# Performance work log

Measured on AMD Instinct MI355X. Metric: run time of the kernel, lower is better.

## Reference

```python
import jax, jax.numpy as jnp
import numpy as np

B, N, DIM = 1, 4096, 512
HEADS, LOCAL_HEADS = 8, 4           # int(8*0.6)=4 local, 4 content
CONTENT_HEADS = HEADS - LOCAL_HEADS
HEAD_DIM = DIM // HEADS             # 64
WINDOW = 64                         # == H == W so window attention is well-formed
TOPK_RATIO = 0.2
SCALE = HEAD_DIM ** -0.5


def _window_partition(x, ws):
    Bb, H, W, C = x.shape
    pad_h = (ws - H % ws) % ws
    pad_w = (ws - W % ws) % ws
    x = jnp.pad(x, ((0, 0), (0, pad_h), (0, pad_w), (0, 0)))
    Hp, Wp = H + pad_h, W + pad_w
    x = x.reshape(Bb, Hp // ws, ws, Wp // ws, ws, C)
    win = x.transpose(0, 1, 3, 2, 4, 5).reshape(-1, ws, ws, C)
    return win, (Hp, Wp)


def _window_unpartition(win, ws, pad_hw, hw):
    Hp, Wp = pad_hw
    H, W = hw
    Bb = win.shape[0] // (Hp * Wp // ws // ws)
    x = win.reshape(Bb, Hp // ws, Wp // ws, ws, ws, -1)
    x = x.transpose(0, 1, 3, 2, 4, 5).reshape(Bb, Hp, Wp, -1)
    return x[:, :H, :W, :]


def setup_inputs() -> dict:
    key = jax.random.key(0)
    ks = jax.random.split(key, 12)
    s = 0.02
    f32 = jnp.float32
    ld = LOCAL_HEADS * HEAD_DIM      # 256
    cd = CONTENT_HEADS * HEAD_DIM    # 256
    return {
        'x': jax.random.normal(ks[0], (B, N, DIM), f32),
        'W_lqkv': jax.random.normal(ks[1], (DIM, 3 * ld), f32) * s,
        'b_lqkv': jnp.zeros((3 * ld,), f32),
        'W_cqkv': jax.random.normal(ks[2], (DIM, 3 * cd), f32) * s,
        'b_cqkv': jnp.zeros((3 * cd,), f32),
        'W_lproj': jax.random.normal(ks[3], (ld, DIM), f32) * s,
        'b_lproj': jnp.zeros((DIM,), f32),
        'W_cproj': jax.random.normal(ks[4], (cd, DIM), f32) * s,
        'b_cproj': jnp.zeros((DIM,), f32),
        'W_s1': jax.random.normal(ks[5], (DIM, DIM // 2), f32) * s,
        'b_s1': jnp.zeros((DIM // 2,), f32),
        'W_s2': jax.random.normal(ks[6], (DIM // 2, 1), f32) * s,
        'b_s2': jnp.zeros((1,), f32),
    }


def reference(x, W_lqkv, b_lqkv, W_cqkv, b_cqkv, W_lproj, b_lproj,
              W_cproj, b_cproj, W_s1, b_s1, W_s2, b_s2):
    Bb, Nn, C = x.shape
    H = W = int(np.sqrt(Nn))

    # ---- local (windowed) attention branch ----
    x_sp = x.reshape(Bb, H, W, C)
    x_win, pad_hw = _window_partition(x_sp, WINDOW)           # (Bw, ws, ws, C)
    Bw, Hw, Ww, _ = x_win.shape
    Nw = Hw * Ww
    xl = x_win.reshape(Bw, Nw, C)
    lqkv = (xl @ W_lqkv + b_lqkv).reshape(Bw, Nw, 3, LOCAL_HEADS, HEAD_DIM)
    lqkv = lqkv.transpose(2, 0, 3, 1, 4)                      # (3, Bw, h, Nw, d)
    lq, lk, lv = lqkv[0], lqkv[1], lqkv[2]
    lattn = jnp.einsum('bhqd,bhkd->bhqk', lq, lk) * SCALE
    lattn = jax.nn.softmax(lattn, axis=-1)
    lo = jnp.einsum('bhqk,bhkd->bhqd', lattn, lv)
    lo = lo.transpose(0, 2, 1, 3).reshape(Bw, Hw, Ww, LOCAL_HEADS * HEAD_DIM)
    lo = _window_unpartition(lo, WINDOW, pad_hw, (H, W)).reshape(Bb, Nn, -1)
    local_x = lo @ W_lproj + b_lproj

    # ---- saliency-gated content-based sparse attention branch ----
    h = jax.nn.gelu(x @ W_s1 + b_s1, approximate=False)
    scores = (h @ W_s2 + b_s2)[..., 0]                        # (B, N)
    K = max(1, int(Nn * TOPK_RATIO))
    _, idx = jax.lax.top_k(scores, K)                         # (B, K)
    mask = jnp.zeros((Bb, Nn), bool).at[jnp.arange(Bb)[:, None], idx].set(True)

    cqkv = (x @ W_cqkv + b_cqkv).reshape(Bb, Nn, 3, CONTENT_HEADS, HEAD_DIM)
    cqkv = cqkv.transpose(2, 0, 3, 1, 4)
    cq, ck, cv = cqkv[0], cqkv[1], cqkv[2]
    cattn = jnp.einsum('bhqd,bhkd->bhqk', cq, ck) * SCALE
    cattn = jnp.where(mask[:, None, None, :], cattn, -jnp.inf)
    cattn = jax.nn.softmax(cattn, axis=-1)
    co = jnp.einsum('bhqk,bhkd->bhqd', cattn, cv)
    co = co.transpose(0, 2, 1, 3).reshape(Bb, Nn, CONTENT_HEADS * HEAD_DIM)
    content_x = co @ W_cproj + b_cproj

    out = local_x + content_x
    attn = jnp.concatenate([lattn.mean(axis=1), cattn.mean(axis=1)], axis=1)
    return out, attn
```

## Files before the change

kernel.cpp:

```cpp
#include <hip/hip_runtime.h>

typedef __bf16 bf16;
typedef __bf16 bf16x8 __attribute__((ext_vector_type(8)));
typedef float  floatx4 __attribute__((ext_vector_type(4)));

__device__ __forceinline__ floatx4 mfma16(bf16x8 a, bf16x8 b, floatx4 c) {
    return __builtin_amdgcn_mfma_f32_16x16x32_bf16(a, b, c, 0, 0, 0);
}

__global__ void k_transpose(const float* __restrict__ src, bf16* __restrict__ dst,
                            int R, int C) {
    __shared__ float tile[32][33];
    int c0 = blockIdx.x * 32, r0 = blockIdx.y * 32;
    int tx = threadIdx.x, ty = threadIdx.y;
    for (int i = ty; i < 32; i += 8) {
        int r = r0 + i, c = c0 + tx;
        tile[i][tx] = (r < R && c < C) ? src[r * C + c] : 0.f;
    }
    __syncthreads();
    for (int i = ty; i < 32; i += 8) {
        int r = r0 + tx, c = c0 + i;
        if (r < R && c < C) dst[(size_t)c * R + r] = (bf16)tile[tx][i];
    }
}

__global__ __launch_bounds__(256) void k_xcast(const float* __restrict__ x,
                                               bf16* __restrict__ xb) {
    int i = (blockIdx.x * 256 + threadIdx.x) * 8;
    float4 f0 = *(const float4*)(x + i);
    float4 f1 = *(const float4*)(x + i + 4);
    bf16x8 a;
    a[0] = (bf16)f0.x; a[1] = (bf16)f0.y; a[2] = (bf16)f0.z; a[3] = (bf16)f0.w;
    a[4] = (bf16)f1.x; a[5] = (bf16)f1.y; a[6] = (bf16)f1.z; a[7] = (bf16)f1.w;
    *(bf16x8*)(xb + i) = a;
}

__global__ __launch_bounds__(256) void k_vtr(const bf16* __restrict__ src,
                                             bf16* __restrict__ dst, int R) {
    __shared__ bf16 tile[64][66];
    int t = threadIdx.x;
    int tr = blockIdx.x, h = blockIdx.y;
    const bf16* s = src + ((size_t)h * R + tr * 64) * 64;
    #pragma unroll
    for (int rr = 0; rr < 16; ++rr) {
        int row = rr * 4 + (t >> 6);
        tile[row][t & 63] = s[row * 64 + (t & 63)];
    }
    __syncthreads();
    bf16* d = dst + (size_t)h * 64 * R + tr * 64;
    #pragma unroll
    for (int cc = 0; cc < 16; ++cc) {
        int col = cc * 4 + (t >> 6);
        d[(size_t)col * R + (t & 63)] = tile[t & 63][col];
    }
}

__global__ __launch_bounds__(256) void k_qkv(
    const bf16* __restrict__ xb,
    const bf16* __restrict__ WlT, const bf16* __restrict__ WcT,
    const float* __restrict__ b_l, const float* __restrict__ b_c,
    bf16* __restrict__ lq, bf16* __restrict__ lk, bf16* __restrict__ lv,
    bf16* __restrict__ cq, bf16* __restrict__ ck, bf16* __restrict__ cv)
{
    const int tid = threadIdx.x;
    const int wave = tid >> 6, lane = tid & 63;
    const int ln15 = lane & 15, quad = lane >> 4;
    const int m0 = blockIdx.x * 64 + wave * 16;
    const int n0 = blockIdx.y * 64;

    floatx4 acc[4];
    for (int s = 0; s < 4; ++s) acc[s] = (floatx4){0.f, 0.f, 0.f, 0.f};

    for (int k0 = 0; k0 < 512; k0 += 32) {
        bf16x8 a = *(const bf16x8*)(xb + (m0 + ln15) * 512 + k0 + quad * 8);
        for (int s = 0; s < 4; ++s) {
            int cg = n0 + s * 16 + ln15;
            const bf16* bt = (cg < 768) ? (WlT + cg * 512) : (WcT + (cg - 768) * 512);
            bf16x8 b = *(const bf16x8*)(bt + k0 + quad * 8);
            acc[s] = mfma16(a, b, acc[s]);
        }
    }

    for (int s = 0; s < 4; ++s) {
        int cg = n0 + s * 16 + ln15;
        for (int r = 0; r < 4; ++r) {
            int row = m0 + quad * 4 + r;
            float v = acc[s][r];
            if (cg < 768) {
                v += b_l[cg];
                int qkv = cg >> 8, hh = (cg >> 6) & 3, d = cg & 63;
                if (qkv == 0)      lq[(hh * 4096 + row) * 64 + d] = (bf16)(v * 0.125f);
                else if (qkv == 1) lk[(hh * 4096 + row) * 64 + d] = (bf16)v;
                else               lv[(hh * 4096 + row) * 64 + d] = (bf16)v;
            } else {
                int c = cg - 768;
                v += b_c[c];
                int qkv = c >> 8, hh = (c >> 6) & 3, d = c & 63;
                if (qkv == 0)      cq[(hh * 4096 + row) * 64 + d] = (bf16)(v * 0.125f);
                else if (qkv == 1) ck[(hh * 4096 + row) * 64 + d] = (bf16)v;
                else               cv[(hh * 4096 + row) * 64 + d] = (bf16)v;
            }
        }
    }
}

__global__ __launch_bounds__(256) void k_scores(
    const float* __restrict__ x, const float* __restrict__ Ws1,
    const float* __restrict__ bs1, const float* __restrict__ Ws2,
    const float* __restrict__ bs2, float* __restrict__ scores)
{
    __shared__ float xs[4][512];
    int row0 = blockIdx.x * 4;
    int t = threadIdx.x;
    for (int i = t; i < 512; i += 256) {
        int r = i >> 7, k4 = (i & 127) * 4;
        *(float4*)&xs[r][k4] = *(const float4*)&x[(row0 + r) * 512 + k4];
    }
    __syncthreads();
    int r = t >> 6, cb = (t & 63) * 4;
    float acc[4] = {0.f, 0.f, 0.f, 0.f};
    #pragma unroll 4
    for (int k = 0; k < 512; ++k) {
        float a = xs[r][k];
        float4 w = *(const float4*)(Ws1 + k * 256 + cb);
        acc[0] = fmaf(a, w.x, acc[0]); acc[1] = fmaf(a, w.y, acc[1]);
        acc[2] = fmaf(a, w.z, acc[2]); acc[3] = fmaf(a, w.w, acc[3]);
    }
    float s = 0.f;
    for (int j = 0; j < 4; ++j) {
        float v = acc[j] + bs1[cb + j];
        float g = 0.5f * v * (1.0f + erff(v * 0.70710678118654752f));
        s = fmaf(g, Ws2[cb + j], s);
    }
    s += __shfl_xor(s, 1, 64);  s += __shfl_xor(s, 2, 64);
    s += __shfl_xor(s, 4, 64);  s += __shfl_xor(s, 8, 64);
    s += __shfl_xor(s, 16, 64); s += __shfl_xor(s, 32, 64);
    if ((t & 63) == 0) scores[row0 + r] = s + bs2[0];
}

__global__ __launch_bounds__(1024) void k_topk(const float* __restrict__ scores,
                                               int* __restrict__ sel, int* __restrict__ pos) {
    __shared__ unsigned ubuf[4096];
    __shared__ unsigned cga[2048], cgb[2048];
    __shared__ int bidx[1024];
    __shared__ int ctr, bctr, Bbin;
    int tid = threadIdx.x;
    if (tid == 0) { ctr = 0; bctr = 0; }
    for (int i = tid; i < 2048; i += 1024) cga[i] = 0u;
    __syncthreads();
    for (int i = tid; i < 4096; i += 1024) {
        unsigned s = __float_as_uint(scores[i]);
        unsigned u = (s & 0x80000000u) ? ~s : (s | 0x80000000u);
        ubuf[i] = u;
        pos[i] = -1;
        atomicAdd(&cga[u >> 21], 1u);
    }
    __syncthreads();
    unsigned* src = cga; unsigned* dst = cgb;
    for (int off = 1; off < 2048; off <<= 1) {
        for (int i = tid; i < 2048; i += 1024)
            dst[i] = src[i] + ((i + off < 2048) ? src[i + off] : 0u);
        __syncthreads();
        unsigned* tmp = src; src = dst; dst = tmp;
    }
    for (int b = tid; b < 2048; b += 1024) {
        unsigned ge = src[b];
        unsigned gt = (b < 2047) ? src[b + 1] : 0u;
        if (ge >= 819u && gt < 819u) Bbin = b;
    }
    __syncthreads();
    int B = Bbin;
    int countAbove = (B < 2047) ? (int)src[B + 1] : 0;
    int need = 819 - countAbove;
    for (int i = tid; i < 4096; i += 1024) {
        int b = (int)(ubuf[i] >> 21);
        if (b > B) {
            int slot = atomicAdd(&ctr, 1);
            sel[slot] = i;
            pos[i] = slot;
        } else if (b == B) {
            int ls = atomicAdd(&bctr, 1);
            if (ls < 1024) bidx[ls] = i;
        }
    }
    __syncthreads();
    int m = bctr;
    if (m <= 1024) {
        for (int e = tid; e < m; e += 1024) {
            int i = bidx[e];
            unsigned ui = ubuf[i];
            int rank = 0;
            for (int j = 0; j < m; ++j) {
                int ij = bidx[j];
                unsigned uj = ubuf[ij];
                rank += (uj > ui || (uj == ui && ij < i)) ? 1 : 0;
            }
            if (rank < need) { int slot = countAbove + rank; sel[slot] = i; pos[i] = slot; }
        }
    } else {
        for (int i = tid; i < 4096; i += 1024) {
            if ((int)(ubuf[i] >> 21) != B) continue;
            unsigned ui = ubuf[i];
            int rank = 0;
            for (int j = 0; j < 4096; ++j) {
                if ((int)(ubuf[j] >> 21) != B) continue;
                unsigned uj = ubuf[j];
                rank += (uj > ui || (uj == ui && j < i)) ? 1 : 0;
            }
            if (rank < need) { int slot = countAbove + rank; sel[slot] = i; pos[i] = slot; }
        }
    }
}

__global__ __launch_bounds__(256) void k_gather(
    const bf16* __restrict__ ck, const bf16* __restrict__ cv,
    const int* __restrict__ sel,
    bf16* __restrict__ ckg, bf16* __restrict__ cvg)
{
    int g = blockIdx.x * 4 + (threadIdx.x >> 6);
    int d = threadIdx.x & 63;
    int hh = g / 896, r = g % 896;
    int src = (r < 819) ? sel[r] : -1;
    bf16 kv = (src >= 0) ? ck[(hh * 4096 + src) * 64 + d] : (bf16)0.0f;
    bf16 vv = (src >= 0) ? cv[(hh * 4096 + src) * 64 + d] : (bf16)0.0f;
    ckg[(hh * 896 + r) * 64 + d] = kv;
    cvg[(hh * 896 + r) * 64 + d] = vv;
}

__global__ __launch_bounds__(256, 5) void k_pass2b(
    const bf16* __restrict__ lq, const bf16* __restrict__ lk, const bf16* __restrict__ lvT,
    const bf16* __restrict__ cq, const bf16* __restrict__ ckg, const bf16* __restrict__ cvgT,
    float* __restrict__ partOL,
    float* __restrict__ partOC,
    float* __restrict__ partSL,
    float* __restrict__ partSC)
{
    __shared__ __align__(16) bf16 pbuf[4][2][16 * 40];
    int wave = threadIdx.x >> 6, lane = threadIdx.x & 63;
    int ln15 = lane & 15, quad = lane >> 4;
    int m0 = blockIdx.x * 64 + wave * 16;
    int y = blockIdx.y;
    bool local = y < 32;
    int h     = local ? (y >> 3) : ((y - 32) >> 1);
    int split = local ? (y & 7) : ((y - 32) & 1);
    int NV    = local ? 4096 : 896;
    int kbeg  = local ? split * 512 : split * 448;
    int kcnt  = local ? 512 : 448;

    const bf16* Qh = (local ? lq : cq) + (h * 4096 + m0) * 64;
    const bf16* Kh = (local ? lk : ckg) + h * NV * 64;
    const bf16* Vh = (local ? lvT : cvgT) + h * 64 * NV;

    bf16x8 af0 = *(const bf16x8*)(Qh + ln15 * 64 + quad * 8);
    bf16x8 af1 = *(const bf16x8*)(Qh + ln15 * 64 + 32 + quad * 8);

    floatx4 o[4];
    #pragma unroll
    for (int ds = 0; ds < 4; ++ds) o[ds] = (floatx4){0.f, 0.f, 0.f, 0.f};
    float se[4] = {0.f, 0.f, 0.f, 0.f};

    for (int key0 = kbeg; key0 < kbeg + kcnt; key0 += 64) {
        #pragma unroll
        for (int c = 0; c < 2; ++c) {
            int kb = key0 + c * 32;
            bf16* pb = &pbuf[wave][c][0];
            #pragma unroll
            for (int s = 0; s < 2; ++s) {
                int kc = kb + s * 16;
                const bf16* krow = Kh + (kc + ln15) * 64;
                floatx4 z0 = (floatx4){0.f, 0.f, 0.f, 0.f};
                floatx4 z1 = (floatx4){0.f, 0.f, 0.f, 0.f};
                z0 = mfma16(af0, *(const bf16x8*)(krow + quad * 8), z0);
                z1 = mfma16(af1, *(const bf16x8*)(krow + 32 + quad * 8), z1);
                bool valid = local || (kc + ln15) < 819;
                #pragma unroll
                for (int r = 0; r < 4; ++r) {
                    float p = valid ? __expf(fminf(z0[r] + z1[r], 60.f)) : 0.0f;
                    se[r] += p;
                    pb[(quad * 4 + r) * 40 + s * 16 + ln15] = (bf16)p;
                }
            }
        }
        #pragma unroll
        for (int c = 0; c < 2; ++c) {
            int kb = key0 + c * 32;
            bf16x8 ap = *(const bf16x8*)(&pbuf[wave][c][0] + ln15 * 40 + quad * 8);
            #pragma unroll
            for (int ds = 0; ds < 4; ++ds) {
                const bf16* vrow = Vh + (ds * 16 + ln15) * NV + kb + quad * 8;
                o[ds] = mfma16(ap, *(const bf16x8*)vrow, o[ds]);
            }
        }
    }

    float* ps = (local ? partSL : partSC) + (split * 4 + h) * 4096;
    #pragma unroll
    for (int r = 0; r < 4; ++r) {
        float s = se[r];
        s += __shfl_xor(s, 1, 64);
        s += __shfl_xor(s, 2, 64);
        s += __shfl_xor(s, 4, 64);
        s += __shfl_xor(s, 8, 64);
        if (ln15 == 0) ps[m0 + quad * 4 + r] = s;
    }

    float* ob = (local ? partOL : partOC) + (size_t)split * (4096 * 256);
    #pragma unroll
    for (int ds = 0; ds < 4; ++ds)
        for (int r = 0; r < 4; ++r)
            ob[(m0 + quad * 4 + r) * 256 + h * 64 + ds * 16 + ln15] = o[ds][r];
}

__global__ __launch_bounds__(256) void k_reduce2(
    const float* __restrict__ partOL, const float* __restrict__ partOC,
    const float* __restrict__ partSL, const float* __restrict__ partSC,
    float* __restrict__ lsum, float* __restrict__ lo, float* __restrict__ co)
{
    int t = threadIdx.x;
    int q0 = blockIdx.x * 4;
    int r = t >> 6, cc = (t & 63) * 4;
    int q = q0 + r;
    int h = cc >> 6;

    float sl = 0.f;
    #pragma unroll
    for (int s = 0; s < 8; ++s) sl += partSL[(s * 4 + h) * 4096 + q];
    float rll = 1.0f / fmaxf(sl, 1e-30f);
    float a0 = 0.f, a1 = 0.f, a2 = 0.f, a3 = 0.f;
    #pragma unroll
    for (int s = 0; s < 8; ++s) {
        float4 v = *(const float4*)(partOL + (size_t)s * 1048576 + q * 256 + cc);
        a0 += v.x; a1 += v.y; a2 += v.z; a3 += v.w;
    }
    *(float4*)(lo + q * 256 + cc) = (float4){a0 * rll, a1 * rll, a2 * rll, a3 * rll};

    float sc = partSC[h * 4096 + q] + partSC[(4 + h) * 4096 + q];
    float rlc = 1.0f / fmaxf(sc, 1e-30f);
    float4 v0 = *(const float4*)(partOC + q * 256 + cc);
    float4 v1 = *(const float4*)(partOC + 1048576 + q * 256 + cc);
    *(float4*)(co + q * 256 + cc) = (float4){(v0.x + v1.x) * rlc, (v0.y + v1.y) * rlc,
                                             (v0.z + v1.z) * rlc, (v0.w + v1.w) * rlc};

    if (t < 32) {
        int h8 = t >> 2, rr = t & 3, qq = q0 + rr;
        float s = 0.f;
        if (h8 < 4) {
            #pragma unroll
            for (int sp = 0; sp < 8; ++sp) s += partSL[(sp * 4 + h8) * 4096 + qq];
        } else {
            s = partSC[(h8 - 4) * 4096 + qq] + partSC[(4 + h8 - 4) * 4096 + qq];
        }
        lsum[h8 * 4096 + qq] = s;
    }
}

__global__ __launch_bounds__(256) void k_pass2a(
    const bf16* __restrict__ lq, const bf16* __restrict__ lk,
    const bf16* __restrict__ cq, const bf16* __restrict__ ckg,
    const float* __restrict__ lsum,
    float* __restrict__ attn_local,
    bf16* __restrict__ pcomp)
{
    int wave = threadIdx.x >> 6, lane = threadIdx.x & 63;
    int ln15 = lane & 15, quad = lane >> 4;
    int m0 = blockIdx.x * 64 + wave * 16;
    int y = blockIdx.y;
    bool local = y < 32;
    const bf16* Q  = local ? lq : cq;
    const bf16* Kt = local ? lk : ckg;
    int NV = local ? 4096 : 896;
    int kbeg = local ? y * 128 : (y - 32) * 128;
    int kend = kbeg + 128;
    int hbase = local ? 0 : 4;

    bf16x8 af[4][2];
    #pragma unroll
    for (int h2 = 0; h2 < 4; ++h2)
        for (int ks = 0; ks < 2; ++ks)
            af[h2][ks] = *(const bf16x8*)(Q + (h2 * 4096 + m0 + ln15) * 64 + ks * 32 + quad * 8);

    float rl[4][4];
    #pragma unroll
    for (int h2 = 0; h2 < 4; ++h2)
        for (int r = 0; r < 4; ++r)
            rl[h2][r] = 0.25f / fmaxf(lsum[(hbase + h2) * 4096 + m0 + quad * 4 + r], 1e-30f);

    for (int key0 = kbeg; key0 < kend; key0 += 32) {
        float pm[2][4] = {{0.f, 0.f, 0.f, 0.f}, {0.f, 0.f, 0.f, 0.f}};
        #pragma unroll
        for (int h2 = 0; h2 < 4; ++h2) {
            #pragma unroll
            for (int s = 0; s < 2; ++s) {
                int kc = key0 + s * 16;
                const bf16* krow = Kt + (h2 * NV + kc + ln15) * 64;
                floatx4 z0 = (floatx4){0.f, 0.f, 0.f, 0.f};
                floatx4 z1 = (floatx4){0.f, 0.f, 0.f, 0.f};
                z0 = mfma16(af[h2][0], *(const bf16x8*)(krow + quad * 8), z0);
                z1 = mfma16(af[h2][1], *(const bf16x8*)(krow + 32 + quad * 8), z1);
                bool valid = local || (kc + ln15) < 819;
                if (valid)
                    for (int r = 0; r < 4; ++r)
                        pm[s][r] += __expf(fminf(z0[r] + z1[r], 60.f)) * rl[h2][r];
            }
        }
        if (local) {
            #pragma unroll
            for (int s = 0; s < 2; ++s)
                for (int r = 0; r < 4; ++r)
                    attn_local[(m0 + quad * 4 + r) * 4096 + key0 + s * 16 + ln15] = pm[s][r];
        } else {
            #pragma unroll
            for (int s = 0; s < 2; ++s) {
                int kc = key0 + s * 16 + ln15;
                if (kc < 832)
                    for (int r = 0; r < 4; ++r)
                        pcomp[(m0 + quad * 4 + r) * 832 + kc] = (bf16)(pm[s][r]);
            }
        }
    }
}

__global__ __launch_bounds__(256) void k_expand(const bf16* __restrict__ pcomp,
                                                const int* __restrict__ pos,
                                                float* __restrict__ attn_content) {
    int row = blockIdx.x;
    int c0 = threadIdx.x * 16;
    const bf16* prow = pcomp + row * 832;
    float vals[16];
    #pragma unroll
    for (int j = 0; j < 16; ++j) {
        int p = pos[c0 + j];
        vals[j] = (p >= 0) ? (float)prow[p] : 0.0f;
    }
    float* dst = attn_content + (size_t)row * 4096 + c0;
    *(float4*)(dst)      = (float4){vals[0], vals[1], vals[2], vals[3]};
    *(float4*)(dst + 4)  = (float4){vals[4], vals[5], vals[6], vals[7]};
    *(float4*)(dst + 8)  = (float4){vals[8], vals[9], vals[10], vals[11]};
    *(float4*)(dst + 12) = (float4){vals[12], vals[13], vals[14], vals[15]};
}

__global__ __launch_bounds__(256) void k_proj(
    const float* __restrict__ lo, const float* __restrict__ co,
    const bf16* __restrict__ WlpT, const bf16* __restrict__ WcpT,
    const float* __restrict__ bl, const float* __restrict__ bc,
    float* __restrict__ out)
{
    const int tid = threadIdx.x;
    const int wave = tid >> 6, lane = tid & 63;
    const int ln15 = lane & 15, quad = lane >> 4;
    const int m0 = blockIdx.x * 64 + wave * 16;
    const int n0 = blockIdx.y * 64;

    floatx4 acc[4];
    for (int s = 0; s < 4; ++s) acc[s] = (floatx4){0.f, 0.f, 0.f, 0.f};

    for (int k0 = 0; k0 < 256; k0 += 32) {
        const float* lp = lo + (m0 + ln15) * 256 + k0 + quad * 8;
        const float* cp = co + (m0 + ln15) * 256 + k0 + quad * 8;
        float4 l0 = *(const float4*)lp, l1 = *(const float4*)(lp + 4);
        float4 c0 = *(const float4*)cp, c1 = *(const float4*)(cp + 4);
        bf16x8 al, ac;
        al[0] = (bf16)l0.x; al[1] = (bf16)l0.y; al[2] = (bf16)l0.z; al[3] = (bf16)l0.w;
        al[4] = (bf16)l1.x; al[5] = (bf16)l1.y; al[6] = (bf16)l1.z; al[7] = (bf16)l1.w;
        ac[0] = (bf16)c0.x; ac[1] = (bf16)c0.y; ac[2] = (bf16)c0.z; ac[3] = (bf16)c0.w;
        ac[4] = (bf16)c1.x; ac[5] = (bf16)c1.y; ac[6] = (bf16)c1.z; ac[7] = (bf16)c1.w;
        for (int s = 0; s < 4; ++s) {
            int c = n0 + s * 16 + ln15;
            acc[s] = mfma16(al, *(const bf16x8*)(WlpT + c * 256 + k0 + quad * 8), acc[s]);
            acc[s] = mfma16(ac, *(const bf16x8*)(WcpT + c * 256 + k0 + quad * 8), acc[s]);
        }
    }
    for (int s = 0; s < 4; ++s) {
        int c = n0 + s * 16 + ln15;
        float bias = bl[c] + bc[c];
        for (int r = 0; r < 4; ++r)
            out[(m0 + quad * 4 + r) * 512 + c] = acc[s][r] + bias;
    }
}

#define OFF_WLQKVT  0L
#define OFF_WCQKVT  786432L
#define OFF_LQ      1572864L
#define OFF_LK      3670016L
#define OFF_LVT     5767168L
#define OFF_CQ      7864320L
#define OFF_CK      9961472L
#define OFF_CV      12058624L
#define OFF_PCOMP   9961472L
#define OFF_CKG     16777216L
#define OFF_CVGT    17235968L
#define OFF_WLPT    16777216L
#define OFF_WCPT    17039360L
#define OFF_SCORES  17694720L
#define OFF_SEL     17711104L
#define OFF_POS     17715200L
#define OFF_LSUM    17731584L
#define OFF_LO      17862656L
#define OFF_CO      22056960L
#define WS_TOTAL    26251264L

extern "C" void kernel_launch(void* const* d_in, const int* in_sizes, int n_in,
                              void* d_out, int out_size, void* d_ws, size_t ws_size,
                              hipStream_t stream) {
    if (ws_size < (size_t)WS_TOTAL) return;

    const float* x       = (const float*)d_in[0];
    const float* W_lqkv  = (const float*)d_in[1];
    const float* b_lqkv  = (const float*)d_in[2];
    const float* W_cqkv  = (const float*)d_in[3];
    const float* b_cqkv  = (const float*)d_in[4];
    const float* W_lproj = (const float*)d_in[5];
    const float* b_lproj = (const float*)d_in[6];
    const float* W_cproj = (const float*)d_in[7];
    const float* b_cproj = (const float*)d_in[8];
    const float* W_s1    = (const float*)d_in[9];
    const float* b_s1    = (const float*)d_in[10];
    const float* W_s2    = (const float*)d_in[11];
    const float* b_s2    = (const float*)d_in[12];

    char* ws = (char*)d_ws;
    bf16* WlqkvT  = (bf16*)(ws + OFF_WLQKVT);
    bf16* WcqkvT  = (bf16*)(ws + OFF_WCQKVT);
    bf16* lq    = (bf16*)(ws + OFF_LQ);
    bf16* lk    = (bf16*)(ws + OFF_LK);
    bf16* lvT   = (bf16*)(ws + OFF_LVT);
    bf16* cq    = (bf16*)(ws + OFF_CQ);
    bf16* ck    = (bf16*)(ws + OFF_CK);
    bf16* cv    = (bf16*)(ws + OFF_CV);
    bf16* pcomp = (bf16*)(ws + OFF_PCOMP);
    bf16* ckg   = (bf16*)(ws + OFF_CKG);
    bf16* cvgT  = (bf16*)(ws + OFF_CVGT);
    bf16* WlpT  = (bf16*)(ws + OFF_WLPT);
    bf16* WcpT  = (bf16*)(ws + OFF_WCPT);
    float* scores  = (float*)(ws + OFF_SCORES);
    int*   sel     = (int*)(ws + OFF_SEL);
    int*   pos     = (int*)(ws + OFF_POS);
    float* lsum    = (float*)(ws + OFF_LSUM);
    float* lo      = (float*)(ws + OFF_LO);
    float* co      = (float*)(ws + OFF_CO);
    bf16*  xb      = (bf16*)(ws + OFF_LO);
    bf16*  lv      = (bf16*)(ws + OFF_CO);
    bf16*  cvg     = (bf16*)(ws + OFF_CO + 2097152);

    float* outp = (float*)d_out;
    float* attn_local   = outp + 2097152;
    float* attn_content = attn_local + 4096 * 4096;
    float* partOL = attn_content;
    float* partOC = attn_content + 8388608;
    float* partSL = attn_content + 10485760;
    float* partSC = attn_content + 10616832;

    k_transpose<<<dim3(24, 16), dim3(32, 8), 0, stream>>>(W_lqkv, WlqkvT, 512, 768);
    k_transpose<<<dim3(24, 16), dim3(32, 8), 0, stream>>>(W_cqkv, WcqkvT, 512, 768);
    k_xcast<<<1024, 256, 0, stream>>>(x, xb);

    k_qkv<<<dim3(64, 24), 256, 0, stream>>>(xb, WlqkvT, WcqkvT, b_lqkv, b_cqkv,
                                            lq, lk, lv, cq, ck, cv);
    k_vtr<<<dim3(64, 4), 256, 0, stream>>>(lv, lvT, 4096);
    k_scores<<<1024, 256, 0, stream>>>(x, W_s1, b_s1, W_s2, b_s2, scores);
    k_topk<<<1, 1024, 0, stream>>>(scores, sel, pos);
    k_gather<<<896, 256, 0, stream>>>(ck, cv, sel, ckg, cvg);
    k_vtr<<<dim3(14, 4), 256, 0, stream>>>(cvg, cvgT, 896);
    k_pass2b<<<dim3(64, 40), 256, 0, stream>>>(lq, lk, lvT, cq, ckg, cvgT,
                                               partOL, partOC, partSL, partSC);
    k_reduce2<<<1024, 256, 0, stream>>>(partOL, partOC, partSL, partSC, lsum, lo, co);
    k_pass2a<<<dim3(64, 39), 256, 0, stream>>>(lq, lk, cq, ckg, lsum,
                                               attn_local, pcomp);
    k_transpose<<<dim3(16, 8), dim3(32, 8), 0, stream>>>(W_lproj, WlpT, 256, 512);
    k_transpose<<<dim3(16, 8), dim3(32, 8), 0, stream>>>(W_cproj, WcpT, 256, 512);
    k_expand<<<4096, 256, 0, stream>>>(pcomp, pos, attn_content);
    k_proj<<<dim3(64, 8), 256, 0, stream>>>(lo, co, WlpT, WcpT, b_lproj, b_cproj, outp);
}
```

Baseline: 648.9 us.

## Fuse small prep kernels, store attention outputs as bf16, batch score rows

Merges the weight transposes and x cast into one prep launch, fuses the gather with the V transposes, and folds the projection-weight transposes into the expand kernel, which cuts the number of kernel launches. The reduce kernel now writes its local and content outputs in bf16, so the projection reads half the bytes and skips the conversion. The saliency-score kernel computes 16 rows per block so each loaded weight is reused across 4 rows. The projection uses narrower column tiles to launch more blocks, at some cost in redundant A loads.

```diff
diff --git a/kernel.cpp b/kernel.cpp
--- a/kernel.cpp
+++ b/kernel.cpp
@@ -1,6 +1,7 @@
 #include <hip/hip_runtime.h>
 
 typedef __bf16 bf16;
+typedef __bf16 bf16x4 __attribute__((ext_vector_type(4)));
 typedef __bf16 bf16x8 __attribute__((ext_vector_type(8)));
 typedef float  floatx4 __attribute__((ext_vector_type(4)));
 
@@ -8,11 +9,13 @@
     return __builtin_amdgcn_mfma_f32_16x16x32_bf16(a, b, c, 0, 0, 0);
 }
 
-__global__ void k_transpose(const float* __restrict__ src, bf16* __restrict__ dst,
-                            int R, int C) {
-    __shared__ float tile[32][33];
-    int c0 = blockIdx.x * 32, r0 = blockIdx.y * 32;
-    int tx = threadIdx.x, ty = threadIdx.y;
+__device__ __forceinline__ void transpose_tile(const float* __restrict__ src,
+                                               bf16* __restrict__ dst,
+                                               int R, int C, int rt, int ct,
+                                               float (*tile)[33]) {
+    int t = threadIdx.x;
+    int tx = t & 31, ty = t >> 5;
+    int c0 = ct * 32, r0 = rt * 32;
     for (int i = ty; i < 32; i += 8) {
         int r = r0 + i, c = c0 + tx;
         tile[i][tx] = (r < R && c < C) ? src[r * C + c] : 0.f;
@@ -24,34 +27,25 @@
     }
 }
 
-__global__ __launch_bounds__(256) void k_xcast(const float* __restrict__ x,
-                                               bf16* __restrict__ xb) {
-    int i = (blockIdx.x * 256 + threadIdx.x) * 8;
-    float4 f0 = *(const float4*)(x + i);
-    float4 f1 = *(const float4*)(x + i + 4);
-    bf16x8 a;
-    a[0] = (bf16)f0.x; a[1] = (bf16)f0.y; a[2] = (bf16)f0.z; a[3] = (bf16)f0.w;
-    a[4] = (bf16)f1.x; a[5] = (bf16)f1.y; a[6] = (bf16)f1.z; a[7] = (bf16)f1.w;
-    *(bf16x8*)(xb + i) = a;
-}
-
-__global__ __launch_bounds__(256) void k_vtr(const bf16* __restrict__ src,
-                                             bf16* __restrict__ dst, int R) {
-    __shared__ bf16 tile[64][66];
-    int t = threadIdx.x;
-    int tr = blockIdx.x, h = blockIdx.y;
-    const bf16* s = src + ((size_t)h * R + tr * 64) * 64;
-    #pragma unroll
-    for (int rr = 0; rr < 16; ++rr) {
-        int row = rr * 4 + (t >> 6);
-        tile[row][t & 63] = s[row * 64 + (t & 63)];
-    }
-    __syncthreads();
-    bf16* d = dst + (size_t)h * 64 * R + tr * 64;
-    #pragma unroll
-    for (int cc = 0; cc < 16; ++cc) {
-        int col = cc * 4 + (t >> 6);
-        d[(size_t)col * R + (t & 63)] = tile[t & 63][col];
+__global__ __launch_bounds__(256) void k_prep(
+    const float* __restrict__ W_lqkv, const float* __restrict__ W_cqkv,
+    const float* __restrict__ x,
+    bf16* __restrict__ WlT, bf16* __restrict__ WcT, bf16* __restrict__ xb)
+{
+    __shared__ float tile[32][33];
+    int b = blockIdx.x;
+    if (b < 384) {
+        transpose_tile(W_lqkv, WlT, 512, 768, b / 24, b % 24, tile);
+    } else if (b < 768) {
+        transpose_tile(W_cqkv, WcT, 512, 768, (b - 384) / 24, (b - 384) % 24, tile);
+    } else {
+        int i = ((b - 768) * 256 + threadIdx.x) * 8;
+        float4 f0 = *(const float4*)(x + i);
+        float4 f1 = *(const float4*)(x + i + 4);
+        bf16x8 a;
+        a[0] = (bf16)f0.x; a[1] = (bf16)f0.y; a[2] = (bf16)f0.z; a[3] = (bf16)f0.w;
+        a[4] = (bf16)f1.x; a[5] = (bf16)f1.y; a[6] = (bf16)f1.z; a[7] = (bf16)f1.w;
+        *(bf16x8*)(xb + i) = a;
     }
 }
 
@@ -109,33 +103,47 @@
     const float* __restrict__ bs1, const float* __restrict__ Ws2,
     const float* __restrict__ bs2, float* __restrict__ scores)
 {
-    __shared__ float xs[4][512];
-    int row0 = blockIdx.x * 4;
+    __shared__ float xs[16][512];
+    int row0 = blockIdx.x * 16;
     int t = threadIdx.x;
-    for (int i = t; i < 512; i += 256) {
+    for (int i = t; i < 2048; i += 256) {
         int r = i >> 7, k4 = (i & 127) * 4;
         *(float4*)&xs[r][k4] = *(const float4*)&x[(row0 + r) * 512 + k4];
     }
     __syncthreads();
-    int r = t >> 6, cb = (t & 63) * 4;
-    float acc[4] = {0.f, 0.f, 0.f, 0.f};
-    #pragma unroll 4
+    int w = t >> 6, cb = (t & 63) * 4;
+    float acc[4][4];
+    #pragma unroll
+    for (int rr = 0; rr < 4; ++rr)
+        for (int j = 0; j < 4; ++j) acc[rr][j] = 0.f;
+    #pragma unroll 2
     for (int k = 0; k < 512; ++k) {
-        float a = xs[r][k];
-        float4 w = *(const float4*)(Ws1 + k * 256 + cb);
-        acc[0] = fmaf(a, w.x, acc[0]); acc[1] = fmaf(a, w.y, acc[1]);
-        acc[2] = fmaf(a, w.z, acc[2]); acc[3] = fmaf(a, w.w, acc[3]);
-    }
-    float s = 0.f;
-    for (int j = 0; j < 4; ++j) {
-        float v = acc[j] + bs1[cb + j];
-        float g = 0.5f * v * (1.0f + erff(v * 0.70710678118654752f));
-        s = fmaf(g, Ws2[cb + j], s);
-    }
-    s += __shfl_xor(s, 1, 64);  s += __shfl_xor(s, 2, 64);
-    s += __shfl_xor(s, 4, 64);  s += __shfl_xor(s, 8, 64);
-    s += __shfl_xor(s, 16, 64); s += __shfl_xor(s, 32, 64);
-    if ((t & 63) == 0) scores[row0 + r] = s + bs2[0];
+        float4 wv = *(const float4*)(Ws1 + k * 256 + cb);
+        #pragma unroll
+        for (int rr = 0; rr < 4; ++rr) {
+            float a = xs[w * 4 + rr][k];
+            acc[rr][0] = fmaf(a, wv.x, acc[rr][0]);
+            acc[rr][1] = fmaf(a, wv.y, acc[rr][1]);
+            acc[rr][2] = fmaf(a, wv.z, acc[rr][2]);
+            acc[rr][3] = fmaf(a, wv.w, acc[rr][3]);
+        }
+    }
+    float b1[4] = {bs1[cb], bs1[cb + 1], bs1[cb + 2], bs1[cb + 3]};
+    float w2[4] = {Ws2[cb], Ws2[cb + 1], Ws2[cb + 2], Ws2[cb + 3]};
+    #pragma unroll
+    for (int rr = 0; rr < 4; ++rr) {
+        float s = 0.f;
+        #pragma unroll
+        for (int j = 0; j < 4; ++j) {
+            float v = acc[rr][j] + b1[j];
+            float g = 0.5f * v * (1.0f + erff(v * 0.70710678118654752f));
+            s = fmaf(g, w2[j], s);
+        }
+        s += __shfl_xor(s, 1, 64);  s += __shfl_xor(s, 2, 64);
+        s += __shfl_xor(s, 4, 64);  s += __shfl_xor(s, 8, 64);
+        s += __shfl_xor(s, 16, 64); s += __shfl_xor(s, 32, 64);
+        if ((t & 63) == 0) scores[row0 + w * 4 + rr] = s + bs2[0];
+    }
 }
 
 __global__ __launch_bounds__(1024) void k_topk(const float* __restrict__ scores,
@@ -212,19 +220,52 @@
     }
 }
 
-__global__ __launch_bounds__(256) void k_gather(
+__global__ __launch_bounds__(256) void k_vt2(
+    const bf16* __restrict__ lv, bf16* __restrict__ lvT,
     const bf16* __restrict__ ck, const bf16* __restrict__ cv,
     const int* __restrict__ sel,
-    bf16* __restrict__ ckg, bf16* __restrict__ cvg)
-{
-    int g = blockIdx.x * 4 + (threadIdx.x >> 6);
-    int d = threadIdx.x & 63;
-    int hh = g / 896, r = g % 896;
-    int src = (r < 819) ? sel[r] : -1;
-    bf16 kv = (src >= 0) ? ck[(hh * 4096 + src) * 64 + d] : (bf16)0.0f;
-    bf16 vv = (src >= 0) ? cv[(hh * 4096 + src) * 64 + d] : (bf16)0.0f;
-    ckg[(hh * 896 + r) * 64 + d] = kv;
-    cvg[(hh * 896 + r) * 64 + d] = vv;
+    bf16* __restrict__ ckg, bf16* __restrict__ cvgT)
+{
+    __shared__ bf16 tile[64][66];
+    int b = blockIdx.x;
+    int t = threadIdx.x;
+    int lane = t & 63, grp = t >> 6;
+    if (b < 256) {
+        int tr = b & 63, h = b >> 6;
+        const bf16* s = lv + ((size_t)h * 4096 + tr * 64) * 64;
+        #pragma unroll
+        for (int rr = 0; rr < 16; ++rr) {
+            int row = rr * 4 + grp;
+            tile[row][lane] = s[row * 64 + lane];
+        }
+        __syncthreads();
+        bf16* d = lvT + (size_t)h * 64 * 4096 + tr * 64;
+        #pragma unroll
+        for (int cc = 0; cc < 16; ++cc) {
+            int col = cc * 4 + grp;
+            d[(size_t)col * 4096 + lane] = tile[lane][col];
+        }
+    } else {
+        int g = b - 256;
+        int hh = g / 14, tl = g % 14;
+        int r0 = tl * 64;
+        #pragma unroll
+        for (int rr = 0; rr < 16; ++rr) {
+            int row = r0 + rr * 4 + grp;
+            int src = (row < 819) ? sel[row] : -1;
+            bf16 kv = (src >= 0) ? ck[(hh * 4096 + src) * 64 + lane] : (bf16)0.0f;
+            bf16 vv = (src >= 0) ? cv[(hh * 4096 + src) * 64 + lane] : (bf16)0.0f;
+            ckg[(hh * 896 + row) * 64 + lane] = kv;
+            tile[rr * 4 + grp][lane] = vv;
+        }
+        __syncthreads();
+        bf16* d = cvgT + (size_t)hh * 64 * 896 + r0;
+        #pragma unroll
+        for (int cc = 0; cc < 16; ++cc) {
+            int col = cc * 4 + grp;
+            d[(size_t)col * 896 + lane] = tile[lane][col];
+        }
+    }
 }
 
 __global__ __launch_bounds__(256, 5) void k_pass2b(
@@ -314,7 +355,7 @@
 __global__ __launch_bounds__(256) void k_reduce2(
     const float* __restrict__ partOL, const float* __restrict__ partOC,
     const float* __restrict__ partSL, const float* __restrict__ partSC,
-    float* __restrict__ lsum, float* __restrict__ lo, float* __restrict__ co)
+    float* __restrict__ lsum, bf16* __restrict__ lob, bf16* __restrict__ cob)
 {
     int t = threadIdx.x;
     int q0 = blockIdx.x * 4;
@@ -332,14 +373,19 @@
         float4 v = *(const float4*)(partOL + (size_t)s * 1048576 + q * 256 + cc);
         a0 += v.x; a1 += v.y; a2 += v.z; a3 += v.w;
     }
-    *(float4*)(lo + q * 256 + cc) = (float4){a0 * rll, a1 * rll, a2 * rll, a3 * rll};
+    bf16x4 ol;
+    ol[0] = (bf16)(a0 * rll); ol[1] = (bf16)(a1 * rll);
+    ol[2] = (bf16)(a2 * rll); ol[3] = (bf16)(a3 * rll);
+    *(bf16x4*)(lob + q * 256 + cc) = ol;
 
     float sc = partSC[h * 4096 + q] + partSC[(4 + h) * 4096 + q];
     float rlc = 1.0f / fmaxf(sc, 1e-30f);
     float4 v0 = *(const float4*)(partOC + q * 256 + cc);
     float4 v1 = *(const float4*)(partOC + 1048576 + q * 256 + cc);
-    *(float4*)(co + q * 256 + cc) = (float4){(v0.x + v1.x) * rlc, (v0.y + v1.y) * rlc,
-                                             (v0.z + v1.z) * rlc, (v0.w + v1.w) * rlc};
+    bf16x4 oc;
+    oc[0] = (bf16)((v0.x + v1.x) * rlc); oc[1] = (bf16)((v0.y + v1.y) * rlc);
+    oc[2] = (bf16)((v0.z + v1.z) * rlc); oc[3] = (bf16)((v0.w + v1.w) * rlc);
+    *(bf16x4*)(cob + q * 256 + cc) = oc;
 
     if (t < 32) {
         int h8 = t >> 2, rr = t & 3, qq = q0 + rr;
@@ -420,27 +466,39 @@
     }
 }
 
-__global__ __launch_bounds__(256) void k_expand(const bf16* __restrict__ pcomp,
-                                                const int* __restrict__ pos,
-                                                float* __restrict__ attn_content) {
-    int row = blockIdx.x;
-    int c0 = threadIdx.x * 16;
-    const bf16* prow = pcomp + row * 832;
-    float vals[16];
-    #pragma unroll
-    for (int j = 0; j < 16; ++j) {
-        int p = pos[c0 + j];
-        vals[j] = (p >= 0) ? (float)prow[p] : 0.0f;
-    }
-    float* dst = attn_content + (size_t)row * 4096 + c0;
-    *(float4*)(dst)      = (float4){vals[0], vals[1], vals[2], vals[3]};
-    *(float4*)(dst + 4)  = (float4){vals[4], vals[5], vals[6], vals[7]};
-    *(float4*)(dst + 8)  = (float4){vals[8], vals[9], vals[10], vals[11]};
-    *(float4*)(dst + 12) = (float4){vals[12], vals[13], vals[14], vals[15]};
+__global__ __launch_bounds__(256) void k_expand2(
+    const bf16* __restrict__ pcomp, const int* __restrict__ pos,
+    const float* __restrict__ W_lproj, const float* __restrict__ W_cproj,
+    bf16* __restrict__ WlpT, bf16* __restrict__ WcpT,
+    float* __restrict__ attn_content)
+{
+    __shared__ float tile[32][33];
+    int b = blockIdx.x;
+    if (b < 4096) {
+        int c0 = threadIdx.x * 16;
+        const bf16* prow = pcomp + b * 832;
+        float vals[16];
+        #pragma unroll
+        for (int j = 0; j < 16; ++j) {
+            int p = pos[c0 + j];
+            vals[j] = (p >= 0) ? (float)prow[p] : 0.0f;
+        }
+        float* dst = attn_content + (size_t)b * 4096 + c0;
+        *(float4*)(dst)      = (float4){vals[0], vals[1], vals[2], vals[3]};
+        *(float4*)(dst + 4)  = (float4){vals[4], vals[5], vals[6], vals[7]};
+        *(float4*)(dst + 8)  = (float4){vals[8], vals[9], vals[10], vals[11]};
+        *(float4*)(dst + 12) = (float4){vals[12], vals[13], vals[14], vals[15]};
+    } else if (b < 4224) {
+        int g = b - 4096;
+        transpose_tile(W_lproj, WlpT, 256, 512, g / 16, g % 16, tile);
+    } else {
+        int g = b - 4224;
+        transpose_tile(W_cproj, WcpT, 256, 512, g / 16, g % 16, tile);
+    }
 }
 
 __global__ __launch_bounds__(256) void k_proj(
-    const float* __restrict__ lo, const float* __restrict__ co,
+    const bf16* __restrict__ lob, const bf16* __restrict__ cob,
     const bf16* __restrict__ WlpT, const bf16* __restrict__ WcpT,
     const float* __restrict__ bl, const float* __restrict__ bc,
     float* __restrict__ out)
@@ -449,28 +507,24 @@
     const int wave = tid >> 6, lane = tid & 63;
     const int ln15 = lane & 15, quad = lane >> 4;
     const int m0 = blockIdx.x * 64 + wave * 16;
-    const int n0 = blockIdx.y * 64;
-
-    floatx4 acc[4];
-    for (int s = 0; s < 4; ++s) acc[s] = (floatx4){0.f, 0.f, 0.f, 0.f};
+    const int n0 = blockIdx.y * 32;
+
+    floatx4 acc[2];
+    acc[0] = (floatx4){0.f, 0.f, 0.f, 0.f};
+    acc[1] = (floatx4){0.f, 0.f, 0.f, 0.f};
 
     for (int k0 = 0; k0 < 256; k0 += 32) {
-        const float* lp = lo + (m0 + ln15) * 256 + k0 + quad * 8;
-        const float* cp = co + (m0 + ln15) * 256 + k0 + quad * 8;
-        float4 l0 = *(const float4*)lp, l1 = *(const float4*)(lp + 4);
-        float4 c0 = *(const float4*)cp, c1 = *(const float4*)(cp + 4);
-        bf16x8 al, ac;
-        al[0] = (bf16)l0.x; al[1] = (bf16)l0.y; al[2] = (bf16)l0.z; al[3] = (bf16)l0.w;
-        al[4] = (bf16)l1.x; al[5] = (bf16)l1.y; al[6] = (bf16)l1.z; al[7] = (bf16)l1.w;
-        ac[0] = (bf16)c0.x; ac[1] = (bf16)c0.y; ac[2] = (bf16)c0.z; ac[3] = (bf16)c0.w;
-        ac[4] = (bf16)c1.x; ac[5] = (bf16)c1.y; ac[6] = (bf16)c1.z; ac[7] = (bf16)c1.w;
-        for (int s = 0; s < 4; ++s) {
+        bf16x8 al = *(const bf16x8*)(lob + (m0 + ln15) * 256 + k0 + quad * 8);
+        bf16x8 ac = *(const bf16x8*)(cob + (m0 + ln15) * 256 + k0 + quad * 8);
+        #pragma unroll
+        for (int s = 0; s < 2; ++s) {
             int c = n0 + s * 16 + ln15;
             acc[s] = mfma16(al, *(const bf16x8*)(WlpT + c * 256 + k0 + quad * 8), acc[s]);
             acc[s] = mfma16(ac, *(const bf16x8*)(WcpT + c * 256 + k0 + quad * 8), acc[s]);
         }
     }
-    for (int s = 0; s < 4; ++s) {
+    #pragma unroll
+    for (int s = 0; s < 2; ++s) {
         int c = n0 + s * 16 + ln15;
         float bias = bl[c] + bc[c];
         for (int r = 0; r < 4; ++r)
@@ -536,11 +590,10 @@
     int*   sel     = (int*)(ws + OFF_SEL);
     int*   pos     = (int*)(ws + OFF_POS);
     float* lsum    = (float*)(ws + OFF_LSUM);
-    float* lo      = (float*)(ws + OFF_LO);
-    float* co      = (float*)(ws + OFF_CO);
     bf16*  xb      = (bf16*)(ws + OFF_LO);
+    bf16*  lob     = (bf16*)(ws + OFF_LO);
     bf16*  lv      = (bf16*)(ws + OFF_CO);
-    bf16*  cvg     = (bf16*)(ws + OFF_CO + 2097152);
+    bf16*  cob     = (bf16*)(ws + OFF_CO);
 
     float* outp = (float*)d_out;
     float* attn_local   = outp + 2097152;
@@ -550,24 +603,18 @@
     float* partSL = attn_content + 10485760;
     float* partSC = attn_content + 10616832;
 
-    k_transpose<<<dim3(24, 16), dim3(32, 8), 0, stream>>>(W_lqkv, WlqkvT, 512, 768);
-    k_transpose<<<dim3(24, 16), dim3(32, 8), 0, stream>>>(W_cqkv, WcqkvT, 512, 768);
-    k_xcast<<<1024, 256, 0, stream>>>(x, xb);
-
+    k_prep<<<1792, 256, 0, stream>>>(W_lqkv, W_cqkv, x, WlqkvT, WcqkvT, xb);
     k_qkv<<<dim3(64, 24), 256, 0, stream>>>(xb, WlqkvT, WcqkvT, b_lqkv, b_cqkv,
                                             lq, lk, lv, cq, ck, cv);
-    k_vtr<<<dim3(64, 4), 256, 0, stream>>>(lv, lvT, 4096);
-    k_scores<<<1024, 256, 0, stream>>>(x, W_s1, b_s1, W_s2, b_s2, scores);
+    k_scores<<<256, 256, 0, stream>>>(x, W_s1, b_s1, W_s2, b_s2, scores);
     k_topk<<<1, 1024, 0, stream>>>(scores, sel, pos);
-    k_gather<<<896, 256, 0, stream>>>(ck, cv, sel, ckg, cvg);
-    k_vtr<<<dim3(14, 4), 256, 0, stream>>>(cvg, cvgT, 896);
+    k_vt2<<<312, 256, 0, stream>>>(lv, lvT, ck, cv, sel, ckg, cvgT);
     k_pass2b<<<dim3(64, 40), 256, 0, stream>>>(lq, lk, lvT, cq, ckg, cvgT,
                                                partOL, partOC, partSL, partSC);
-    k_reduce2<<<1024, 256, 0, stream>>>(partOL, partOC, partSL, partSC, lsum, lo, co);
+    k_reduce2<<<1024, 256, 0, stream>>>(partOL, partOC, partSL, partSC, lsum, lob, cob);
     k_pass2a<<<dim3(64, 39), 256, 0, stream>>>(lq, lk, cq, ckg, lsum,
                                                attn_local, pcomp);
-    k_transpose<<<dim3(16, 8), dim3(32, 8), 0, stream>>>(W_lproj, WlpT, 256, 512);
-    k_transpose<<<dim3(16, 8), dim3(32, 8), 0, stream>>>(W_cproj, WcpT, 256, 512);
-    k_expand<<<4096, 256, 0, stream>>>(pcomp, pos, attn_content);
-    k_proj<<<dim3(64, 8), 256, 0, stream>>>(lo, co, WlpT, WcpT, b_lproj, b_cproj, outp);
-}
+    k_expand2<<<4352, 256, 0, stream>>>(pcomp, pos, W_lproj, W_cproj,
+                                        WlpT, WcpT, attn_content);
+    k_proj<<<dim3(64, 16), 256, 0, stream>>>(lob, cob, WlpT, WcpT, b_lproj, b_cproj, outp);
+}
```

Measured after the change: 679.8 us. +4.8%, slower.
